# Kernel optimization log

Hardware: AMD Instinct MI355X
Metric: run time of the kernel (lower is better)

The kernel has to match this reference:

```python
import jax, jax.numpy as jnp
import numpy as np

DIM = 512
NUM_HEADS = 8
HEAD_DIM = DIM // NUM_HEADS
REL_POS_BINS = 961
B, N = 64, 256


def setup_inputs() -> dict:
    key = jax.random.key(0)
    ks = jax.random.split(key, 7)
    x = jax.random.normal(ks[0], (B, N, DIM), dtype=jnp.float32)
    rel_pos_index = jax.random.randint(ks[1], (N, N), 0, REL_POS_BINS)
    s = 1.0 / np.sqrt(DIM)
    qkv_w = jax.random.normal(ks[2], (3 * DIM, DIM), dtype=jnp.float32) * s
    qkv_b = jax.random.normal(ks[3], (3 * DIM,), dtype=jnp.float32) * 0.02
    proj_w = jax.random.normal(ks[4], (DIM, DIM), dtype=jnp.float32) * s
    proj_b = jax.random.normal(ks[5], (DIM,), dtype=jnp.float32) * 0.02
    rel_pos_bias = jax.random.normal(ks[6], (NUM_HEADS, REL_POS_BINS), dtype=jnp.float32) * 0.02
    return {"x": x, "rel_pos_index": rel_pos_index, "qkv_w": qkv_w,
            "qkv_b": qkv_b, "proj_w": proj_w, "proj_b": proj_b,
            "rel_pos_bias": rel_pos_bias}


def reference(x, rel_pos_index, qkv_w, qkv_b, proj_w, proj_b, rel_pos_bias):
    Bn, Nn, C = x.shape
    H, D = NUM_HEADS, HEAD_DIM
    qkv = x @ qkv_w.T + qkv_b                      # (B,N,3C)
    qkv = qkv.reshape(Bn, Nn, 3, H, D).transpose(2, 0, 3, 1, 4)  # (3,B,H,N,D)
    q, k, v = qkv[0], qkv[1], qkv[2]
    scale = 1.0 / jnp.sqrt(jnp.asarray(D, dtype=x.dtype))
    scores = jnp.einsum('bhnd,bhmd->bhnm', q, k) * scale          # (B,H,N,N)
    bias = rel_pos_bias[:, rel_pos_index]                          # (H,N,N) gather
    scores = scores + bias[None]
    attn = jax.nn.softmax(scores, axis=-1)
    out = jnp.einsum('bhnm,bhmd->bhnd', attn, v)                   # (B,H,N,D)
    out = out.transpose(0, 2, 1, 3).reshape(Bn, Nn, C)
    return out @ proj_w.T + proj_b
```

## Files before the change

### kernel.cpp

```cpp
#include <hip/hip_runtime.h>
#include <stdint.h>

#define DIM 512
#define NHEADS 8
#define HDIM 64
#define NBINS 961
#define BATCH 64
#define SEQ 256
#define NTOK (BATCH*SEQ)
#define BHND (BATCH*NHEADS*SEQ*HDIM)

using bf16x8 = __attribute__((ext_vector_type(8))) short;
using f32x4  = __attribute__((ext_vector_type(4))) float;

__device__ __forceinline__ unsigned short f2bf(float f) {
  unsigned u = __float_as_uint(f);
  u += 0x7FFF + ((u >> 16) & 1);
  return (unsigned short)(u >> 16);
}

__device__ __forceinline__ void async16(const void* g, void* lds) {
  __builtin_amdgcn_global_load_lds(
      (const __attribute__((address_space(1))) unsigned int*)g,
      (__attribute__((address_space(3))) unsigned int*)lds,
      16, 0, 0);
}


__global__ void cast_kernel(const float* __restrict__ in,
                            unsigned short* __restrict__ out, int n4) {
  int i = blockIdx.x * 256 + threadIdx.x;
  if (i >= n4) return;
  float4 f = reinterpret_cast<const float4*>(in)[i];
  ushort4 o;
  o.x = f2bf(f.x); o.y = f2bf(f.y); o.z = f2bf(f.z); o.w = f2bf(f.w);
  reinterpret_cast<ushort4*>(out)[i] = o;
}

__global__ void bias_kernel(const int* __restrict__ idx,
                            const float* __restrict__ rpb,
                            float* __restrict__ bf) {
  int i = blockIdx.x * 256 + threadIdx.x;
  if (i >= NHEADS * SEQ * SEQ) return;
  int h = i >> 16;
  int r = i & 65535;
  int n = r >> 8, m = r & 255;
  bf[(size_t)h * 65536 + n * 256 + (m & 15) * 16 + (m >> 4)] = rpb[h * NBINS + idx[r]];
}


__device__ __forceinline__ void stage_half(const unsigned short* __restrict__ X,
                                           int row0, int kk, char* dst, int t) {
#pragma unroll
  for (int i = 0; i < 2; ++i) {
    int q = i * 512 + t;
    int r = q >> 3, s = q & 7;
    const unsigned short* src = X + (size_t)(row0 + r) * 512 + kk + ((s ^ (r & 7)) << 3);
    async16(src, dst + (size_t)(i * 512 + ((t >> 6) << 6)) * 16);
  }
}

template<int NBW, int EPI>
__global__ __launch_bounds__(512) void gemm8p(
    const unsigned short* __restrict__ A,
    const unsigned short* __restrict__ Bw,
    const float* __restrict__ bias,
    void* __restrict__ outp, int nbn, int cpx) {
  extern __shared__ char gsm[];
  constexpr int BN   = NBW * 64;
  constexpr int BUF  = 32768 + NBW * 8192;
  const int t = threadIdx.x;
  const int lane = t & 63, l15 = lane & 15, lg = lane >> 4;
  const int wv = t >> 6, wm = wv & 1, wn = wv >> 1;
  const int bid = blockIdx.x;
  const int nid = (bid & 7) * cpx + (bid >> 3);
  const int m0 = (nid / nbn) * 256, n0 = (nid % nbn) * BN;

  f32x4 acc[8][NBW];
  const f32x4 fz = {0.f, 0.f, 0.f, 0.f};
#pragma unroll
  for (int a = 0; a < 8; ++a)
#pragma unroll
    for (int b = 0; b < NBW; ++b) acc[a][b] = fz;

  stage_half(A,  m0,       0, gsm,          t);
  stage_half(A,  m0 + 128, 0, gsm + 16384,  t);
  stage_half(Bw, n0,       0, gsm + 32768,  t);
  if (NBW == 4) stage_half(Bw, n0 + 128, 0, gsm + 49152, t);

  int cur = 0;
#pragma unroll 1
  for (int T = 0; T < 8; ++T) {
    char* Ab  = gsm + cur * BUF;
    char* Bb  = Ab + 32768;
    char* nxt = gsm + (cur ^ 1) * BUF;

    __builtin_amdgcn_s_barrier();
    if (T < 7) {
      stage_half(A, m0,       (T + 1) * 64, nxt,         t);
      stage_half(A, m0 + 128, (T + 1) * 64, nxt + 16384, t);
      asm volatile("s_waitcnt vmcnt(4)" ::: "memory");
    } else {
      asm volatile("s_waitcnt vmcnt(0)" ::: "memory");
    }
    __builtin_amdgcn_sched_barrier(0);

#pragma unroll
    for (int ph = 0; ph < 4; ++ph) {
      const int kh = ph >> 1, mh = ph & 1;
      if (ph == 1 && T < 7) stage_half(Bw, n0, (T + 1) * 64, nxt + 32768, t);
      if (NBW == 4 && ph == 2 && T < 7) stage_half(Bw, n0 + 128, (T + 1) * 64, nxt + 49152, t);

      const int sw = ((kh * 4 + lg) ^ (l15 & 7)) * 16;
      bf16x8 av[4], bv[NBW];
#pragma unroll
      for (int mi = 0; mi < 4; ++mi)
        av[mi] = *(const bf16x8*)(Ab + wm * 16384 + (mh * 64 + mi * 16 + l15) * 128 + sw);
#pragma unroll
      for (int ni = 0; ni < NBW; ++ni) {
        int rb = wn * (NBW * 16) + ni * 16 + l15;
        bv[ni] = *(const bf16x8*)(Bb + (rb >> 7) * 16384 + (rb & 127) * 128 + sw);
      }
      asm volatile("s_waitcnt lgkmcnt(0)" ::: "memory");
      __builtin_amdgcn_sched_barrier(0);
      __builtin_amdgcn_s_setprio(1);
#pragma unroll
      for (int mi = 0; mi < 4; ++mi)
#pragma unroll
        for (int ni = 0; ni < NBW; ++ni)
          acc[mh * 4 + mi][ni] =
              __builtin_amdgcn_mfma_f32_16x16x32_bf16(av[mi], bv[ni], acc[mh * 4 + mi][ni], 0, 0, 0);
      __builtin_amdgcn_s_setprio(0);
      __builtin_amdgcn_sched_barrier(0);
    }
    cur ^= 1;
  }

#pragma unroll
  for (int MI = 0; MI < 8; ++MI)
#pragma unroll
    for (int ni = 0; ni < NBW; ++ni)
#pragma unroll
      for (int r = 0; r < 4; ++r) {
        int row = m0 + wm * 128 + MI * 16 + lg * 4 + r;
        int col = n0 + wn * (NBW * 16) + ni * 16 + l15;
        float v = acc[MI][ni][r] + bias[col];
        if (EPI == 0) {
          int which = col >> 9, hd = col & 511;
          int b = row >> 8, n = row & 255;
          ((unsigned short*)outp)[(size_t)which * BHND +
              (((size_t)(b * NHEADS + (hd >> 6)) * SEQ + n) * HDIM) + (hd & 63)] = f2bf(v);
        } else {
          ((float*)outp)[(size_t)row * 512 + col] = v;
        }
      }
}


__global__ __launch_bounds__(256) void attn_kernel(
    const unsigned short* __restrict__ qb,
    const unsigned short* __restrict__ kb,
    const unsigned short* __restrict__ vb,
    const float* __restrict__ biasf,
    unsigned short* __restrict__ aout) {
  extern __shared__ char smem[];
  char* k_s = smem;
  char* v_s = smem + 32768;
  const int t = threadIdx.x, lane = t & 63, w = t >> 6;
  const int l15 = lane & 15, lg = lane >> 4;
  char* P_s = smem + w * 2048;
  const int nid = (blockIdx.x & 7) * 256 + (blockIdx.x >> 3);
  const int bh = nid >> 2, quarter = nid & 3;
  const int h = bh & 7;
  const int b = bh >> 3;
  const int row0 = quarter * 64 + w * 16;
  const size_t base = (size_t)bh * (SEQ * HDIM);

#pragma unroll
  for (int i = 0; i < 8; ++i) {
    int c = i * 256 + t;
    int row = c >> 3, sl = c & 7;
    bf16x8 val = *(const bf16x8*)(kb + base + (size_t)c * 8);
    *(bf16x8*)(k_s + row * 128 + ((sl * 16) ^ ((row & 7) << 4))) = val;
  }
#pragma unroll
  for (int i = 0; i < 8; ++i) {
    int c = i * 256 + t;
    int key = c >> 3, d0 = (c & 7) * 8;
    bf16x8 val = *(const bf16x8*)(vb + base + (size_t)c * 8);
#pragma unroll
    for (int j = 0; j < 8; ++j) {
      int d = d0 + j;
      int term = (((d & 7) ^ ((d >> 3) & 7)) << 4);
      *(short*)(v_s + d * 512 + ((key * 2) ^ term)) = val[j];
    }
  }
  bf16x8 qa[2];
#pragma unroll
  for (int ks = 0; ks < 2; ++ks)
    qa[ks] = *(const bf16x8*)(qb + base + (size_t)(row0 + l15) * 64 + ks * 32 + lg * 8);
  __syncthreads();

  f32x4 accs[16];
  const f32x4 fz = {0.f, 0.f, 0.f, 0.f};
#pragma unroll
  for (int c = 0; c < 16; ++c) accs[c] = fz;
  __builtin_amdgcn_s_setprio(1);
#pragma unroll
  for (int cf = 0; cf < 16; ++cf) {
    int key = cf * 16 + l15;
#pragma unroll
    for (int ks = 0; ks < 2; ++ks) {
      bf16x8 kf = *(const bf16x8*)(k_s + key * 128 + ((lg * 16 + ks * 64) ^ ((key & 7) << 4)));
      accs[cf] = __builtin_amdgcn_mfma_f32_16x16x32_bf16(qa[ks], kf, accs[cf], 0, 0, 0);
    }
  }
  __builtin_amdgcn_s_setprio(0);

  const float* bh_ptr = biasf + (size_t)h * 65536;
#pragma unroll
  for (int r = 0; r < 4; ++r) {
    int n = row0 + lg * 4 + r;
    const f32x4* bp = (const f32x4*)(bh_ptr + n * 256 + l15 * 16);
    f32x4 b0 = bp[0], b1 = bp[1], b2 = bp[2], b3 = bp[3];
#pragma unroll
    for (int cf = 0; cf < 16; ++cf) {
      float bb = (cf < 4) ? b0[cf] : (cf < 8) ? b1[cf - 4] : (cf < 12) ? b2[cf - 8] : b3[cf - 12];
      accs[cf][r] = accs[cf][r] * 0.125f + bb;
    }
  }

  float pinv[4];
#pragma unroll
  for (int r = 0; r < 4; ++r) {
    float m = -1e30f;
#pragma unroll
    for (int cf = 0; cf < 16; ++cf) m = fmaxf(m, accs[cf][r]);
#pragma unroll
    for (int off = 1; off < 16; off <<= 1) m = fmaxf(m, __shfl_xor(m, off, 64));
    float s = 0.f;
#pragma unroll
    for (int cf = 0; cf < 16; ++cf) {
      float p = __expf(accs[cf][r] - m);
      accs[cf][r] = p;
      s += p;
    }
#pragma unroll
    for (int off = 1; off < 16; off <<= 1) s += __shfl_xor(s, off, 64);
    pinv[r] = 1.0f / s;
  }

  __syncthreads();

  f32x4 acco[4];
#pragma unroll
  for (int c2 = 0; c2 < 4; ++c2) acco[c2] = fz;

  for (int ch = 0; ch < 4; ++ch) {
#pragma unroll
    for (int cl = 0; cl < 4; ++cl)
#pragma unroll
      for (int r = 0; r < 4; ++r) {
        int rowl = lg * 4 + r;
        int ml = cl * 16 + l15;
        float p = accs[ch * 4 + cl][r] * pinv[r];
        *(short*)(P_s + rowl * 128 + ((ml * 2) ^ ((rowl & 7) << 4))) = (short)f2bf(p);
      }
#pragma unroll
    for (int ks = 0; ks < 2; ++ks) {
      bf16x8 pa = *(const bf16x8*)(P_s + l15 * 128 + ((lg * 16 + ks * 64) ^ ((l15 & 7) << 4)));
      int keyb = (ch * 64 + ks * 32 + lg * 8) * 2;
      __builtin_amdgcn_s_setprio(1);
#pragma unroll
      for (int df = 0; df < 4; ++df) {
        int d = df * 16 + l15;
        int term = (((d & 7) ^ ((d >> 3) & 7)) << 4);
        bf16x8 vf = *(const bf16x8*)(v_s + d * 512 + (keyb ^ term));
        acco[df] = __builtin_amdgcn_mfma_f32_16x16x32_bf16(pa, vf, acco[df], 0, 0, 0);
      }
      __builtin_amdgcn_s_setprio(0);
    }
  }

#pragma unroll
  for (int df = 0; df < 4; ++df)
#pragma unroll
    for (int r = 0; r < 4; ++r) {
      int n = row0 + lg * 4 + r;
      int d = df * 16 + l15;
      aout[((size_t)(b * SEQ + n)) * DIM + h * HDIM + d] = f2bf(acco[df][r]);
    }
}


extern "C" void kernel_launch(void* const* d_in, const int* in_sizes, int n_in,
                              void* d_out, int out_size, void* d_ws, size_t ws_size,
                              hipStream_t stream) {
  const float* x      = (const float*)d_in[0];
  const int*   rpi    = (const int*)d_in[1];
  const float* qkv_w  = (const float*)d_in[2];
  const float* qkv_b  = (const float*)d_in[3];
  const float* proj_w = (const float*)d_in[4];
  const float* proj_b = (const float*)d_in[5];
  const float* rpb    = (const float*)d_in[6];

  char* ws = (char*)d_ws;
  unsigned short* xb    = (unsigned short*)ws;
  unsigned short* wqkv  = (unsigned short*)(ws + 16777216);
  unsigned short* wproj = (unsigned short*)(ws + 18350080);
  float*          biasf = (float*)         (ws + 18874368);
  unsigned short* qkvb  = (unsigned short*)(ws + 20971520);
  unsigned short* aoutb = (unsigned short*)(ws + 71303168);

  cast_kernel<<<8192, 256, 0, stream>>>(x, xb, 2097152);
  cast_kernel<<<768, 256, 0, stream>>>(qkv_w, wqkv, 196608);
  cast_kernel<<<256, 256, 0, stream>>>(proj_w, wproj, 65536);
  bias_kernel<<<2048, 256, 0, stream>>>(rpi, rpb, biasf);

  gemm8p<4, 0><<<384, 512, 131072, stream>>>(xb, wqkv, qkv_b, (void*)qkvb, 6, 48);

  attn_kernel<<<2048, 256, 65536, stream>>>(qkvb, qkvb + BHND, qkvb + 2 * (size_t)BHND,
                                            biasf, aoutb);

  gemm8p<2, 1><<<256, 512, 98304, stream>>>(aoutb, wproj, proj_b, d_out, 4, 32);
}
```

Baseline: 108.6 us.

## Write V pre-transposed from QKV GEMM, fuse prep kernels, async-load V in attention

The QKV GEMM epilogue now writes V in the transposed, swizzled layout that attention expects. The attention kernel can then copy V straight into LDS with async global-to-LDS loads instead of doing per-element scattered LDS stores. The three cast kernels and the bias-gather kernel are merged into one launch. The GEMM pipeline wait now drains all outstanding loads before the barrier. The P and V swizzle patterns are changed to reduce LDS bank conflicts. The V epilogue writes become scattered 2-byte global stores, and the stricter vmcnt(0) wait may shorten load/compute overlap in the GEMM.

```diff
diff --git a/kernel.cpp b/kernel.cpp
--- a/kernel.cpp
+++ b/kernel.cpp
@@ -27,25 +27,32 @@
 }
 
 
-__global__ void cast_kernel(const float* __restrict__ in,
-                            unsigned short* __restrict__ out, int n4) {
-  int i = blockIdx.x * 256 + threadIdx.x;
-  if (i >= n4) return;
-  float4 f = reinterpret_cast<const float4*>(in)[i];
-  ushort4 o;
-  o.x = f2bf(f.x); o.y = f2bf(f.y); o.z = f2bf(f.z); o.w = f2bf(f.w);
-  reinterpret_cast<ushort4*>(out)[i] = o;
-}
-
-__global__ void bias_kernel(const int* __restrict__ idx,
+__global__ void prep_kernel(const float* __restrict__ x,
+                            const float* __restrict__ qkv_w,
+                            const float* __restrict__ proj_w,
+                            const int* __restrict__ idx,
                             const float* __restrict__ rpb,
+                            unsigned short* __restrict__ xb,
+                            unsigned short* __restrict__ wqkv,
+                            unsigned short* __restrict__ wproj,
                             float* __restrict__ bf) {
-  int i = blockIdx.x * 256 + threadIdx.x;
-  if (i >= NHEADS * SEQ * SEQ) return;
-  int h = i >> 16;
-  int r = i & 65535;
-  int n = r >> 8, m = r & 255;
-  bf[(size_t)h * 65536 + n * 256 + (m & 15) * 16 + (m >> 4)] = rpb[h * NBINS + idx[r]];
+  int bid = blockIdx.x;
+  if (bid < 9216) {
+    const float* in; unsigned short* out; int i;
+    if (bid < 8192)      { in = x;      out = xb;    i = bid * 256 + threadIdx.x; }
+    else if (bid < 8960) { in = qkv_w;  out = wqkv;  i = (bid - 8192) * 256 + threadIdx.x; }
+    else                 { in = proj_w; out = wproj; i = (bid - 8960) * 256 + threadIdx.x; }
+    float4 f = reinterpret_cast<const float4*>(in)[i];
+    ushort4 o;
+    o.x = f2bf(f.x); o.y = f2bf(f.y); o.z = f2bf(f.z); o.w = f2bf(f.w);
+    reinterpret_cast<ushort4*>(out)[i] = o;
+  } else {
+    int i = (bid - 9216) * 256 + threadIdx.x;
+    int h = i >> 16;
+    int r = i & 65535;
+    int n = r >> 8, m = r & 255;
+    bf[(size_t)h * 65536 + n * 256 + (m & 15) * 16 + (m >> 4)] = rpb[h * NBINS + idx[r]];
+  }
 }
 
 
@@ -65,16 +72,17 @@
     const unsigned short* __restrict__ A,
     const unsigned short* __restrict__ Bw,
     const float* __restrict__ bias,
-    void* __restrict__ outp, int nbn, int cpx) {
+    void* __restrict__ outp,
+    unsigned short* __restrict__ vtb,
+    int nbn, int cpx) {
   extern __shared__ char gsm[];
-  constexpr int BN   = NBW * 64;
   constexpr int BUF  = 32768 + NBW * 8192;
   const int t = threadIdx.x;
   const int lane = t & 63, l15 = lane & 15, lg = lane >> 4;
   const int wv = t >> 6, wm = wv & 1, wn = wv >> 1;
   const int bid = blockIdx.x;
   const int nid = (bid & 7) * cpx + (bid >> 3);
-  const int m0 = (nid / nbn) * 256, n0 = (nid % nbn) * BN;
+  const int m0 = (nid / nbn) * 256, n0 = (nid % nbn) * (NBW * 64);
 
   f32x4 acc[8][NBW];
   const f32x4 fz = {0.f, 0.f, 0.f, 0.f};
@@ -95,13 +103,13 @@
     char* Bb  = Ab + 32768;
     char* nxt = gsm + (cur ^ 1) * BUF;
 
+    asm volatile("s_waitcnt vmcnt(0)" ::: "memory");
     __builtin_amdgcn_s_barrier();
+    __builtin_amdgcn_sched_barrier(0);
+
     if (T < 7) {
       stage_half(A, m0,       (T + 1) * 64, nxt,         t);
       stage_half(A, m0 + 128, (T + 1) * 64, nxt + 16384, t);
-      asm volatile("s_waitcnt vmcnt(4)" ::: "memory");
-    } else {
-      asm volatile("s_waitcnt vmcnt(0)" ::: "memory");
     }
     __builtin_amdgcn_sched_barrier(0);
 
@@ -148,8 +156,15 @@
         if (EPI == 0) {
           int which = col >> 9, hd = col & 511;
           int b = row >> 8, n = row & 255;
-          ((unsigned short*)outp)[(size_t)which * BHND +
-              (((size_t)(b * NHEADS + (hd >> 6)) * SEQ + n) * HDIM) + (hd & 63)] = f2bf(v);
+          if (which == 2) {
+            int h = hd >> 6, d = hd & 63;
+            int bh2 = b * NHEADS + h;
+            int byteoff = d * 512 + ((n * 2) ^ ((d & 7) << 4));
+            vtb[(size_t)bh2 * 16384 + (byteoff >> 1)] = f2bf(v);
+          } else {
+            ((unsigned short*)outp)[(size_t)which * BHND +
+                (((size_t)(b * NHEADS + (hd >> 6)) * SEQ + n) * HDIM) + (hd & 63)] = f2bf(v);
+          }
         } else {
           ((float*)outp)[(size_t)row * 512 + col] = v;
         }
@@ -160,7 +175,7 @@
 __global__ __launch_bounds__(256) void attn_kernel(
     const unsigned short* __restrict__ qb,
     const unsigned short* __restrict__ kb,
-    const unsigned short* __restrict__ vb,
+    const char* __restrict__ vtb,
     const float* __restrict__ biasf,
     unsigned short* __restrict__ aout) {
   extern __shared__ char smem[];
@@ -176,30 +191,30 @@
   const int row0 = quarter * 64 + w * 16;
   const size_t base = (size_t)bh * (SEQ * HDIM);
 
+  bf16x8 kreg[8];
+#pragma unroll
+  for (int i = 0; i < 8; ++i)
+    kreg[i] = *(const bf16x8*)(kb + base + (size_t)(i * 256 + t) * 8);
+  bf16x8 qa[2];
+#pragma unroll
+  for (int ks = 0; ks < 2; ++ks)
+    qa[ks] = *(const bf16x8*)(qb + base + (size_t)(row0 + l15) * 64 + ks * 32 + lg * 8);
+  const char* vsrc = vtb + (size_t)bh * 32768;
+#pragma unroll
+  for (int i = 0; i < 8; ++i) {
+    int c = i * 256 + t;
+    async16(vsrc + (size_t)c * 16, v_s + c * 16);
+  }
 #pragma unroll
   for (int i = 0; i < 8; ++i) {
     int c = i * 256 + t;
     int row = c >> 3, sl = c & 7;
-    bf16x8 val = *(const bf16x8*)(kb + base + (size_t)c * 8);
-    *(bf16x8*)(k_s + row * 128 + ((sl * 16) ^ ((row & 7) << 4))) = val;
-  }
-#pragma unroll
-  for (int i = 0; i < 8; ++i) {
-    int c = i * 256 + t;
-    int key = c >> 3, d0 = (c & 7) * 8;
-    bf16x8 val = *(const bf16x8*)(vb + base + (size_t)c * 8);
-#pragma unroll
-    for (int j = 0; j < 8; ++j) {
-      int d = d0 + j;
-      int term = (((d & 7) ^ ((d >> 3) & 7)) << 4);
-      *(short*)(v_s + d * 512 + ((key * 2) ^ term)) = val[j];
-    }
-  }
-  bf16x8 qa[2];
-#pragma unroll
-  for (int ks = 0; ks < 2; ++ks)
-    qa[ks] = *(const bf16x8*)(qb + base + (size_t)(row0 + l15) * 64 + ks * 32 + lg * 8);
-  __syncthreads();
+    *(bf16x8*)(k_s + row * 128 + ((sl * 16) ^ ((row & 7) << 4))) = kreg[i];
+  }
+  asm volatile("s_waitcnt lgkmcnt(0)" ::: "memory");
+  __builtin_amdgcn_sched_barrier(0);
+  __builtin_amdgcn_s_barrier();
+  __builtin_amdgcn_sched_barrier(0);
 
   f32x4 accs[16];
   const f32x4 fz = {0.f, 0.f, 0.f, 0.f};
@@ -263,19 +278,20 @@
       for (int r = 0; r < 4; ++r) {
         int rowl = lg * 4 + r;
         int ml = cl * 16 + l15;
+        int pterm = (((rowl & 7) ^ ((rowl >> 2) & 2)) << 4);
         float p = accs[ch * 4 + cl][r] * pinv[r];
-        *(short*)(P_s + rowl * 128 + ((ml * 2) ^ ((rowl & 7) << 4))) = (short)f2bf(p);
+        *(short*)(P_s + rowl * 128 + ((ml * 2) ^ pterm)) = (short)f2bf(p);
       }
 #pragma unroll
     for (int ks = 0; ks < 2; ++ks) {
-      bf16x8 pa = *(const bf16x8*)(P_s + l15 * 128 + ((lg * 16 + ks * 64) ^ ((l15 & 7) << 4)));
+      int rterm = (((l15 & 7) ^ ((l15 >> 2) & 2)) << 4);
+      bf16x8 pa = *(const bf16x8*)(P_s + l15 * 128 + ((lg * 16 + ks * 64) ^ rterm));
       int keyb = (ch * 64 + ks * 32 + lg * 8) * 2;
       __builtin_amdgcn_s_setprio(1);
 #pragma unroll
       for (int df = 0; df < 4; ++df) {
         int d = df * 16 + l15;
-        int term = (((d & 7) ^ ((d >> 3) & 7)) << 4);
-        bf16x8 vf = *(const bf16x8*)(v_s + d * 512 + (keyb ^ term));
+        bf16x8 vf = *(const bf16x8*)(v_s + d * 512 + (keyb ^ ((d & 7) << 4)));
         acco[df] = __builtin_amdgcn_mfma_f32_16x16x32_bf16(pa, vf, acco[df], 0, 0, 0);
       }
       __builtin_amdgcn_s_setprio(0);
@@ -311,16 +327,15 @@
   float*          biasf = (float*)         (ws + 18874368);
   unsigned short* qkvb  = (unsigned short*)(ws + 20971520);
   unsigned short* aoutb = (unsigned short*)(ws + 71303168);
-
-  cast_kernel<<<8192, 256, 0, stream>>>(x, xb, 2097152);
-  cast_kernel<<<768, 256, 0, stream>>>(qkv_w, wqkv, 196608);
-  cast_kernel<<<256, 256, 0, stream>>>(proj_w, wproj, 65536);
-  bias_kernel<<<2048, 256, 0, stream>>>(rpi, rpb, biasf);
-
-  gemm8p<4, 0><<<384, 512, 131072, stream>>>(xb, wqkv, qkv_b, (void*)qkvb, 6, 48);
-
-  attn_kernel<<<2048, 256, 65536, stream>>>(qkvb, qkvb + BHND, qkvb + 2 * (size_t)BHND,
+  unsigned short* vtb   = qkvb + 2 * (size_t)BHND;
+
+  prep_kernel<<<11264, 256, 0, stream>>>(x, qkv_w, proj_w, rpi, rpb,
+                                         xb, wqkv, wproj, biasf);
+
+  gemm8p<4, 0><<<384, 512, 131072, stream>>>(xb, wqkv, qkv_b, (void*)qkvb, vtb, 6, 48);
+
+  attn_kernel<<<2048, 256, 65536, stream>>>(qkvb, qkvb + BHND, (const char*)vtb,
                                             biasf, aoutb);
 
-  gemm8p<2, 1><<<256, 512, 98304, stream>>>(aoutb, wproj, proj_b, d_out, 4, 32);
-}
+  gemm8p<2, 1><<<256, 512, 98304, stream>>>(aoutb, wproj, proj_b, d_out, nullptr, 4, 32);
+}
```

New measurement: 117.0 us. 7.8% more time.
